# Optimization experiments

Hardware: AMD Instinct MI355X
Metric: run time of the kernel (lower is better)

Reference implementation:

```python
import jax, jax.numpy as jnp
import numpy as np

B, C, H, W = 4, 256, 64, 64
CP = C // 4  # embedding_channels, k=4 hardcoded
# branch index -> (key-stream i, query/value-stream j); streams: 0=t,1=b,2=m
IIDX = np.array([0, 0, 0, 1, 1, 1, 2, 2, 2])  # which stream feeds k
JIDX = np.array([0, 1, 2, 0, 1, 2, 0, 1, 2])  # which stream feeds q and v


def setup_inputs() -> dict:
    key = jax.random.key(0)
    ks = jax.random.split(key, 6)
    scale = 0.05
    return {
        "t": jax.random.normal(ks[0], (B, C, H, W), jnp.float32),
        "b": jax.random.normal(ks[1], (B, C, H, W), jnp.float32),
        "m": jax.random.normal(ks[2], (B, C, H, W), jnp.float32),
        "W_qkv": jax.random.normal(ks[3], (9, C, C), jnp.float32) * scale,
        "W_red": jax.random.normal(ks[4], (9, CP, C), jnp.float32) * scale,
        "W_rec": jax.random.normal(ks[5], (9, C, CP), jnp.float32) * scale,
    }


def _pool(x):
    # ChannelAttention: global avg pool + global max pool -> [B, C']
    return jnp.mean(x, axis=(2, 3)) + jnp.max(x, axis=(2, 3))


def _channel_attention(q, k, v, w_red, w_rec):
    # q,k,v: [B,C,H,W]; w_red: [C',C]; w_rec: [C,C']
    ori = q + k + v
    red = lambda x: jax.nn.relu(jnp.einsum("bchw,ec->behw", x, w_red))
    qr, kr, vr = red(q), red(k), red(v)
    f = _pool(kr)  # key   -> [B,C']
    g = _pool(qr)  # query -> [B,C']
    h = _pool(vr)  # value -> [B,C']
    # s = f^T g : [B,C',C']; softmax over dim=1 (rows), per torch nn.Softmax(dim=1)
    s = f[:, :, None] * g[:, None, :]
    beta = jax.nn.softmax(s, axis=1)
    vout = jnp.einsum("bi,bij->bj", h, beta)  # [B,C']
    # recovery 1x1 conv on [B,C',1,1]; bilinear upsample from 1x1 == broadcast
    o = jax.nn.sigmoid(jnp.einsum("be,ce->bc", vout, w_rec))  # [B,C]
    return o[:, :, None, None] * ori


def reference(t, b, m, W_qkv, W_red, W_rec):
    x = jnp.stack([t, b, m])  # [3,B,C,H,W]
    Wp = W_qkv.reshape(3, 3, C, C)  # [stream, (q,k,v), C_out, C_in]
    proj = jnp.einsum("sbchw,sjec->sjbehw", x, Wp)  # [3,3,B,C,H,W]
    Q, K, V = proj[:, 0], proj[:, 1], proj[:, 2]  # each [3,B,C,H,W]
    q9, k9, v9 = Q[JIDX], K[IIDX], V[JIDX]  # [9,B,C,H,W]
    outs = jax.vmap(_channel_attention)(q9, k9, v9, W_red, W_rec)
    return outs.sum(axis=0)
```

## Files before the change

### kernel.cpp

```cpp
#include <hip/hip_runtime.h>

#define Bn 4
#define Cn 256
#define HWn 4096
#define CPn 64
#define MP 640

typedef unsigned short u16;
typedef unsigned int u32;

using short8  = __attribute__((ext_vector_type(8))) short;
using floatx4 = __attribute__((ext_vector_type(4))) float;

static __device__ __forceinline__ u16 f2bf(float f) {
    union { float f; u32 u; } v; v.f = f;
    u32 r = (v.u + 0x7FFFu + ((v.u >> 16) & 1u)) >> 16;
    return (u16)r;
}

static __device__ __forceinline__ void gld16(const u16* g, u16* l) {
    __builtin_amdgcn_global_load_lds(
        (const __attribute__((address_space(1))) u32*)g,
        (__attribute__((address_space(3))) u32*)l, 16, 0, 0);
}


__global__ __launch_bounds__(256) void prep(
    const float* __restrict__ Tt, const float* __restrict__ Bt, const float* __restrict__ Mt,
    const float* __restrict__ Wqkv, const float* __restrict__ Wred,
    u16* __restrict__ xT, u16* __restrict__ CWp)
{
    __shared__ u16 T[64][72];
    __shared__ float As[16][64];
    __shared__ float Bs[16][64];
    const int t = threadIdx.x;

    if (blockIdx.z < 3) {
        const int s  = blockIdx.z, b = blockIdx.y;
        const int ct = blockIdx.x & 3, hwt = blockIdx.x >> 2;
        const int c0 = ct * 64, hw0 = hwt * 64;
        const float* X = (s == 0 ? Tt : (s == 1 ? Bt : Mt)) + (size_t)b * Cn * HWn;

        const int cl = t >> 2, q = t & 3;
        const float* src = X + (size_t)(c0 + cl) * HWn + hw0 + q * 16;
        #pragma unroll
        for (int u = 0; u < 4; ++u) {
            const float4 v = *(const float4*)(src + u * 4);
            T[cl][q * 16 + u * 4 + 0] = f2bf(v.x);
            T[cl][q * 16 + u * 4 + 1] = f2bf(v.y);
            T[cl][q * 16 + u * 4 + 2] = f2bf(v.z);
            T[cl][q * 16 + u * 4 + 3] = f2bf(v.w);
        }
        __syncthreads();

        const int wl = t >> 2;
        u16* dst = xT + ((size_t)((s * Bn + b) * HWn) + hw0 + wl) * Cn + c0 + q * 16;
        #pragma unroll
        for (int u = 0; u < 2; ++u) {
            u32 w0 = (u32)T[q * 16 + u * 8 + 0][wl] | ((u32)T[q * 16 + u * 8 + 1][wl] << 16);
            u32 w1 = (u32)T[q * 16 + u * 8 + 2][wl] | ((u32)T[q * 16 + u * 8 + 3][wl] << 16);
            u32 w2 = (u32)T[q * 16 + u * 8 + 4][wl] | ((u32)T[q * 16 + u * 8 + 5][wl] << 16);
            u32 w3 = (u32)T[q * 16 + u * 8 + 6][wl] | ((u32)T[q * 16 + u * 8 + 7][wl] << 16);
            uint4 pk = {w0, w1, w2, w3};
            *(uint4*)(dst + u * 8) = pk;
        }
        return;
    }

    const int lin = blockIdx.y * 256 + blockIdx.x;
    if (lin >= 108) return;
    const int c0  = (lin & 3) * 64;
    const int rest = lin >> 2;
    const int y9 = rest % 9, s = rest / 9;
    const int tt = y9 / 3, m3 = y9 % 3;
    const int idx = (tt == 1) ? (3 * s + m3) : (3 * m3 + s);

    const float* A  = Wred + (size_t)idx * CPn * Cn;
    const float* Bm = Wqkv + (size_t)(3 * s + tt) * Cn * Cn;

    const int ty = t >> 4, tx = t & 15;
    float acc[4][4] = {};

    for (int k0 = 0; k0 < Cn; k0 += 16) {
        {
            const int r = t >> 2, eq = (t & 3) * 4;
            const float4 a = *(const float4*)(A + (size_t)r * Cn + k0 + eq);
            As[eq + 0][r] = a.x; As[eq + 1][r] = a.y; As[eq + 2][r] = a.z; As[eq + 3][r] = a.w;
        }
        {
            const int r = t >> 4, cq = (t & 15) * 4;
            *(float4*)(&Bs[r][cq]) = *(const float4*)(Bm + (size_t)(k0 + r) * Cn + c0 + cq);
        }
        __syncthreads();
        #pragma unroll
        for (int k = 0; k < 16; ++k) {
            const float4 a4 = *(const float4*)(&As[k][ty * 4]);
            const float4 b4 = *(const float4*)(&Bs[k][tx * 4]);
            const float a[4] = {a4.x, a4.y, a4.z, a4.w};
            const float bb[4] = {b4.x, b4.y, b4.z, b4.w};
            #pragma unroll
            for (int i = 0; i < 4; ++i)
                #pragma unroll
                for (int j = 0; j < 4; ++j)
                    acc[i][j] = fmaf(a[i], bb[j], acc[i][j]);
        }
        __syncthreads();
    }

    u16* outp = CWp + (size_t)s * MP * Cn;
    #pragma unroll
    for (int i = 0; i < 4; ++i) {
        const int row = tt * 192 + m3 * 64 + ty * 4 + i;
        unsigned long long pk =
            (unsigned long long)f2bf(acc[i][0]) |
            ((unsigned long long)f2bf(acc[i][1]) << 16) |
            ((unsigned long long)f2bf(acc[i][2]) << 32) |
            ((unsigned long long)f2bf(acc[i][3]) << 48);
        *(unsigned long long*)(outp + (size_t)row * Cn + c0 + tx * 4) = pk;
    }
}

#define NSUB 16

__global__ __launch_bounds__(256, 1) void redpool_mfma(
    const u16* __restrict__ xT, const u16* __restrict__ CWp,
    float* __restrict__ Psum, float* __restrict__ Pmax)
{
    const int s   = blockIdx.z;
    const int mt  = blockIdx.x >> 4, nch = blockIdx.x & 15;
    const int m0  = mt * 128;
    const int nbase = nch * 1024;

    const u16* Ap = CWp + (size_t)s * MP * Cn;
    const u16* Bp = xT + (size_t)s * Bn * HWn * Cn;

    __shared__ __align__(16) u16 Bs[2][32 * 512];

    const int t = threadIdx.x;
    const int w = t >> 6, lane = t & 63;
    const int l15 = lane & 15, q = lane >> 4;
    const int wr = w >> 1, wc = w & 1;

    short8 af[4][8];
    {
        const u16* Arow = Ap + (size_t)(m0 + wr * 64 + l15) * Cn + q * 8;
        #pragma unroll
        for (int i = 0; i < 4; ++i)
            #pragma unroll
            for (int kk = 0; kk < 8; ++kk)
                af[i][kk] = *(const short8*)(Arow + (size_t)(i * 16) * Cn + kk * 32);
    }

    auto stageB = [&](int it, int buf) {
        const u16* Bsrc = Bp + (size_t)(nbase + it * 64 + l15) * Cn + q * 8;
        #pragma unroll
        for (int pi = 0; pi < 8; ++pi) {
            const int p = w * 8 + pi;
            gld16(Bsrc + (size_t)((p >> 3) * 16) * Cn + (p & 7) * 32, &Bs[buf][p * 512]);
        }
    };
    stageB(0, 0);

    float rs[4][4] = {};
    float rm[4][4] = {};

    for (int it = 0; it < NSUB; ++it) {
        __syncthreads();
        if (it + 1 < NSUB) stageB(it + 1, (it + 1) & 1);
        const u16* bb = Bs[it & 1];

        floatx4 acc[4][2] = {};
        #pragma unroll
        for (int kk = 0; kk < 8; ++kk) {
            short8 bf[2];
            #pragma unroll
            for (int j = 0; j < 2; ++j)
                bf[j] = *(const short8*)&bb[((wc * 2 + j) * 8 + kk) * 512 + lane * 8];
            #pragma unroll
            for (int i = 0; i < 4; ++i)
                #pragma unroll
                for (int j = 0; j < 2; ++j)
                    acc[i][j] = __builtin_amdgcn_mfma_f32_16x16x32_bf16(af[i][kk], bf[j], acc[i][j], 0, 0, 0);
        }
        #pragma unroll
        for (int i = 0; i < 4; ++i)
            #pragma unroll
            for (int r = 0; r < 4; ++r) {
                const float v0 = fmaxf(acc[i][0][r], 0.f);
                const float v1 = fmaxf(acc[i][1][r], 0.f);
                rs[i][r] += v0 + v1;
                rm[i][r] = fmaxf(rm[i][r], fmaxf(v0, v1));
            }
    }

    #pragma unroll
    for (int i = 0; i < 4; ++i)
        #pragma unroll
        for (int r = 0; r < 4; ++r) {
            #pragma unroll
            for (int off = 1; off < 16; off <<= 1) {
                rs[i][r] += __shfl_xor(rs[i][r], off);
                rm[i][r] = fmaxf(rm[i][r], __shfl_xor(rm[i][r], off));
            }
        }

    __syncthreads();
    float* Lsum = (float*)&Bs[0][0];
    float* Lmax = Lsum + 256;
    if (l15 == 0) {
        #pragma unroll
        for (int i = 0; i < 4; ++i)
            #pragma unroll
            for (int r = 0; r < 4; ++r) {
                const int row = wr * 64 + i * 16 + q * 4 + r;
                Lsum[wc * 128 + row] = rs[i][r];
                Lmax[wc * 128 + row] = rm[i][r];
            }
    }
    __syncthreads();
    if (t < 128) {
        const int R = m0 + t;
        const size_t o = ((size_t)s * MP + R) * 16 + nch;
        Psum[o] = Lsum[t] + Lsum[128 + t];
        Pmax[o] = fmaxf(Lmax[t], Lmax[128 + t]);
    }
}

__global__ __launch_bounds__(64) void attn_small(
    const float* __restrict__ Psum, const float* __restrict__ Pmax,
    float* __restrict__ vout)
{
    const int idx = blockIdx.x / Bn;
    const int bb  = blockIdx.x % Bn;
    __shared__ float ff[CPn], gg[CPn], hh[CPn];
    const int t = threadIdx.x;

    float v[3];
    #pragma unroll
    for (int tt = 0; tt < 3; ++tt) {
        const int s_ = (tt == 1) ? idx / 3 : idx % 3;
        const int m3 = (tt == 1) ? idx % 3 : idx / 3;
        const int R  = tt * 192 + m3 * 64 + t;
        const size_t base = ((size_t)s_ * MP + R) * 16 + bb * 4;
        float sm = 0.f, mx = 0.f;
        #pragma unroll
        for (int u = 0; u < 4; ++u) {
            sm += Psum[base + u];
            mx = fmaxf(mx, Pmax[base + u]);
        }
        v[tt] = sm * (1.0f / HWn) + mx;
    }
    gg[t] = v[0];
    ff[t] = v[1];
    hh[t] = v[2];
    __syncthreads();

    const float gj = gg[t];
    float mx = -1e30f;
    for (int i = 0; i < CPn; ++i) mx = fmaxf(mx, ff[i] * gj);
    float den = 0.f, num = 0.f;
    for (int i = 0; i < CPn; ++i) {
        const float e = expf(ff[i] * gj - mx);
        den += e;
        num += hh[i] * e;
    }
    vout[((size_t)idx * Bn + bb) * CPn + t] = num / den;
}

__global__ __launch_bounds__(256) void build_M(
    const float* __restrict__ Wqkv, const float* __restrict__ Wrec,
    const float* __restrict__ vout, u16* __restrict__ Mm)
{
    const int s = blockIdx.x >> 8, m = blockIdx.x & 255;
    const int b = blockIdx.y;
    const int t = threadIdx.x;
    __shared__ float cc[2];

    if (t < CPn) {
        float d[6];
        #pragma unroll
        for (int j = 0; j < 6; ++j) {
            const int idx = (j < 3) ? (s + 3 * j) : (3 * s + (j - 3));
            d[j] = vout[((size_t)idx * Bn + b) * CPn + t] *
                   Wrec[((size_t)idx * Cn + m) * CPn + t];
        }
        #pragma unroll
        for (int off = 32; off >= 1; off >>= 1)
            #pragma unroll
            for (int j = 0; j < 6; ++j)
                d[j] += __shfl_xor(d[j], off);
        if (t == 0) {
            float cA = 0.f, cK = 0.f;
            #pragma unroll
            for (int j = 0; j < 3; ++j) {
                cA += 1.0f / (1.0f + expf(-d[j]));
                cK += 1.0f / (1.0f + expf(-d[j + 3]));
            }
            cc[0] = cA; cc[1] = cK;
        }
    }
    __syncthreads();
    const float cA = cc[0], cK = cc[1];
    const float wq = Wqkv[((size_t)(3 * s + 0) * Cn + m) * Cn + t];
    const float wk = Wqkv[((size_t)(3 * s + 1) * Cn + m) * Cn + t];
    const float wv = Wqkv[((size_t)(3 * s + 2) * Cn + m) * Cn + t];
    Mm[((size_t)(b * 256 + m)) * 768 + s * 256 + t] = f2bf(cA * (wq + wv) + cK * wk);
}

__global__ __launch_bounds__(256, 1) void final_mfma(
    const u16* __restrict__ xT, const u16* __restrict__ Mm,
    float* __restrict__ out)
{
    const int b  = blockIdx.y;
    const int mt = blockIdx.x >> 5, nt = blockIdx.x & 31;
    const int m0 = mt * 128, n0 = nt * 128;

    __shared__ __align__(16) u16 As[2][32 * 512];
    __shared__ __align__(16) u16 Bs[2][32 * 512];

    const int t = threadIdx.x;
    const int w = t >> 6, lane = t & 63;
    const int l15 = lane & 15, q = lane >> 4;
    const int rb = (w >> 1) * 64, cb = (w & 1) * 64;

    auto stage = [&](int it, int buf) {
        const int k0 = it * 128;
        const int s = k0 >> 8, c0 = k0 & 255;
        const u16* Asrc = Mm + (size_t)(b * 256 + m0 + l15) * 768 + k0 + q * 8;
        const u16* Bsrc = xT + ((size_t)((s * Bn + b) * HWn) + n0 + l15) * Cn + c0 + q * 8;
        #pragma unroll
        for (int pi = 0; pi < 8; ++pi) {
            const int p = w * 8 + pi;
            const size_t roff = (size_t)((p >> 2) * 16);
            gld16(Asrc + roff * 768 + (p & 3) * 32, &As[buf][p * 512]);
            gld16(Bsrc + roff * Cn + (p & 3) * 32, &Bs[buf][p * 512]);
        }
    };
    stage(0, 0);

    floatx4 acc[4][4] = {};

    for (int it = 0; it < 6; ++it) {
        __syncthreads();
        if (it + 1 < 6) stage(it + 1, (it + 1) & 1);
        const u16* as = As[it & 1];
        const u16* bs = Bs[it & 1];
        #pragma unroll
        for (int kk = 0; kk < 4; ++kk) {
            short8 af[4], bf[4];
            #pragma unroll
            for (int i = 0; i < 4; ++i)
                af[i] = *(const short8*)&as[((((w >> 1) * 4 + i) << 2) + kk) * 512 + lane * 8];
            #pragma unroll
            for (int j = 0; j < 4; ++j)
                bf[j] = *(const short8*)&bs[((((w & 1) * 4 + j) << 2) + kk) * 512 + lane * 8];
            #pragma unroll
            for (int i = 0; i < 4; ++i)
                #pragma unroll
                for (int j = 0; j < 4; ++j)
                    acc[i][j] = __builtin_amdgcn_mfma_f32_16x16x32_bf16(af[i], bf[j], acc[i][j], 0, 0, 0);
        }
    }

    #pragma unroll
    for (int i = 0; i < 4; ++i)
        #pragma unroll
        for (int j = 0; j < 4; ++j)
            #pragma unroll
            for (int r = 0; r < 4; ++r) {
                const int row = m0 + rb + i * 16 + q * 4 + r;
                const int col = n0 + cb + j * 16 + l15;
                out[((size_t)(b * 256) + row) * HWn + col] = acc[i][j][r];
            }
}

extern "C" void kernel_launch(void* const* d_in, const int* in_sizes, int n_in,
                              void* d_out, int out_size, void* d_ws, size_t ws_size,
                              hipStream_t stream)
{
    const float* Tt   = (const float*)d_in[0];
    const float* Bt   = (const float*)d_in[1];
    const float* Mt   = (const float*)d_in[2];
    const float* Wqkv = (const float*)d_in[3];
    const float* Wred = (const float*)d_in[4];
    const float* Wrec = (const float*)d_in[5];
    float* out = (float*)d_out;

    unsigned char* p = (unsigned char*)d_ws;
    u16* xT = (u16*)p;            p += (size_t)3 * Bn * HWn * Cn * 2;
    u16* Mm = (u16*)p;            p += (size_t)Bn * 256 * 768 * 2;
    u16* CWp = (u16*)p;           p += (size_t)3 * MP * Cn * 2;
    float* Psum = (float*)p;      p += (size_t)3 * MP * 16 * 4;
    float* Pmax = (float*)p;      p += (size_t)3 * MP * 16 * 4;
    float* vout = (float*)p;      p += (size_t)9 * Bn * CPn * 4;

    prep        <<<dim3(256, Bn, 4), 256, 0, stream>>>(Tt, Bt, Mt, Wqkv, Wred, xT, CWp);
    redpool_mfma<<<dim3(80, 1, 3),   256, 0, stream>>>(xT, CWp, Psum, Pmax);
    attn_small  <<<9 * Bn,            64, 0, stream>>>(Psum, Pmax, vout);
    build_M     <<<dim3(768, Bn),    256, 0, stream>>>(Wqkv, Wrec, vout, Mm);
    final_mfma  <<<dim3(64, Bn),     256, 0, stream>>>(xT, Mm, out);
}
```

Measured before the change: 170.3 us.

## Fuse input bf16 transpose with reduction-pool MFMA into a single pass

Splits the weight-composition GEMM into its own small kernel and merges the fp32-to-bf16 transpose of the inputs with the reduce+ReLU+pool MFMA stage. Each block converts a 128-pixel slice, writes xT for the final stage, and also lays the tile out in LDS panes that feed the MFMAs directly. This removes the global re-read of xT that the separate pool kernel needed. In exchange each block recomputes over all 640 rows with A fragments reloaded from global per tile, and the partial-pool buffers grow to 128 slots, so attn_small does more reduction work. The pool kernel also launches fewer blocks (384 instead of 240 plus the prep grid).

```diff
diff --git a/kernel.cpp b/kernel.cpp
--- a/kernel.cpp
+++ b/kernel.cpp
@@ -25,59 +25,22 @@
 }
 
 
-__global__ __launch_bounds__(256) void prep(
-    const float* __restrict__ Tt, const float* __restrict__ Bt, const float* __restrict__ Mt,
+__global__ __launch_bounds__(256) void compose_red(
     const float* __restrict__ Wqkv, const float* __restrict__ Wred,
-    u16* __restrict__ xT, u16* __restrict__ CWp)
-{
-    __shared__ u16 T[64][72];
+    u16* __restrict__ CWp)
+{
+    const int c0 = blockIdx.x * 64;
+    const int y  = blockIdx.y;
+    const int s  = y / 9, y9 = y % 9;
+    const int tt = y9 / 3, m3 = y9 % 3;
+    const int idx = (tt == 1) ? (3 * s + m3) : (3 * m3 + s);
+
+    const float* A  = Wred + (size_t)idx * CPn * Cn;
+    const float* Bm = Wqkv + (size_t)(3 * s + tt) * Cn * Cn;
+
     __shared__ float As[16][64];
     __shared__ float Bs[16][64];
     const int t = threadIdx.x;
-
-    if (blockIdx.z < 3) {
-        const int s  = blockIdx.z, b = blockIdx.y;
-        const int ct = blockIdx.x & 3, hwt = blockIdx.x >> 2;
-        const int c0 = ct * 64, hw0 = hwt * 64;
-        const float* X = (s == 0 ? Tt : (s == 1 ? Bt : Mt)) + (size_t)b * Cn * HWn;
-
-        const int cl = t >> 2, q = t & 3;
-        const float* src = X + (size_t)(c0 + cl) * HWn + hw0 + q * 16;
-        #pragma unroll
-        for (int u = 0; u < 4; ++u) {
-            const float4 v = *(const float4*)(src + u * 4);
-            T[cl][q * 16 + u * 4 + 0] = f2bf(v.x);
-            T[cl][q * 16 + u * 4 + 1] = f2bf(v.y);
-            T[cl][q * 16 + u * 4 + 2] = f2bf(v.z);
-            T[cl][q * 16 + u * 4 + 3] = f2bf(v.w);
-        }
-        __syncthreads();
-
-        const int wl = t >> 2;
-        u16* dst = xT + ((size_t)((s * Bn + b) * HWn) + hw0 + wl) * Cn + c0 + q * 16;
-        #pragma unroll
-        for (int u = 0; u < 2; ++u) {
-            u32 w0 = (u32)T[q * 16 + u * 8 + 0][wl] | ((u32)T[q * 16 + u * 8 + 1][wl] << 16);
-            u32 w1 = (u32)T[q * 16 + u * 8 + 2][wl] | ((u32)T[q * 16 + u * 8 + 3][wl] << 16);
-            u32 w2 = (u32)T[q * 16 + u * 8 + 4][wl] | ((u32)T[q * 16 + u * 8 + 5][wl] << 16);
-            u32 w3 = (u32)T[q * 16 + u * 8 + 6][wl] | ((u32)T[q * 16 + u * 8 + 7][wl] << 16);
-            uint4 pk = {w0, w1, w2, w3};
-            *(uint4*)(dst + u * 8) = pk;
-        }
-        return;
-    }
-
-    const int lin = blockIdx.y * 256 + blockIdx.x;
-    if (lin >= 108) return;
-    const int c0  = (lin & 3) * 64;
-    const int rest = lin >> 2;
-    const int y9 = rest % 9, s = rest / 9;
-    const int tt = y9 / 3, m3 = y9 % 3;
-    const int idx = (tt == 1) ? (3 * s + m3) : (3 * m3 + s);
-
-    const float* A  = Wred + (size_t)idx * CPn * Cn;
-    const float* Bm = Wqkv + (size_t)(3 * s + tt) * Cn * Cn;
-
     const int ty = t >> 4, tx = t & 15;
     float acc[4][4] = {};
 
@@ -120,109 +83,139 @@
     }
 }
 
-#define NSUB 16
-
-__global__ __launch_bounds__(256, 1) void redpool_mfma(
-    const u16* __restrict__ xT, const u16* __restrict__ CWp,
-    float* __restrict__ Psum, float* __restrict__ Pmax)
+__global__ __launch_bounds__(256, 2) void pass1(
+    const float* __restrict__ Tt, const float* __restrict__ Bt, const float* __restrict__ Mt,
+    const u16* __restrict__ CWp,
+    u16* __restrict__ xT, float* __restrict__ Psum, float* __restrict__ Pmax)
 {
     const int s   = blockIdx.z;
-    const int mt  = blockIdx.x >> 4, nch = blockIdx.x & 15;
-    const int m0  = mt * 128;
-    const int nbase = nch * 1024;
-
+    const int nch = blockIdx.x;
+    const int b   = nch >> 5;
+    const int hwb = (nch & 31) * 128;
+
+    const float* X = (s == 0 ? Tt : (s == 1 ? Bt : Mt)) + (size_t)b * Cn * HWn;
     const u16* Ap = CWp + (size_t)s * MP * Cn;
-    const u16* Bp = xT + (size_t)s * Bn * HWn * Cn;
-
-    __shared__ __align__(16) u16 Bs[2][32 * 512];
+    u16* xTb = xT + (size_t)((s * Bn + b) * HWn) * Cn;
+
+    __shared__ u16 T[64][72];
+    __shared__ __align__(16) u16 panes[32 * 512];
 
     const int t = threadIdx.x;
     const int w = t >> 6, lane = t & 63;
     const int l15 = lane & 15, q = lane >> 4;
-    const int wr = w >> 1, wc = w & 1;
-
-    short8 af[4][8];
+    const int cl = t >> 2, q4 = t & 3;
+
+    float rs[5][2][4] = {};
+    float rm[5][2][4] = {};
+
+    float4 v[2][4];
     {
-        const u16* Arow = Ap + (size_t)(m0 + wr * 64 + l15) * Cn + q * 8;
-        #pragma unroll
-        for (int i = 0; i < 4; ++i)
-            #pragma unroll
-            for (int kk = 0; kk < 8; ++kk)
-                af[i][kk] = *(const short8*)(Arow + (size_t)(i * 16) * Cn + kk * 32);
-    }
-
-    auto stageB = [&](int it, int buf) {
-        const u16* Bsrc = Bp + (size_t)(nbase + it * 64 + l15) * Cn + q * 8;
-        #pragma unroll
-        for (int pi = 0; pi < 8; ++pi) {
-            const int p = w * 8 + pi;
-            gld16(Bsrc + (size_t)((p >> 3) * 16) * Cn + (p & 7) * 32, &Bs[buf][p * 512]);
-        }
-    };
-    stageB(0, 0);
-
-    float rs[4][4] = {};
-    float rm[4][4] = {};
-
-    for (int it = 0; it < NSUB; ++it) {
-        __syncthreads();
-        if (it + 1 < NSUB) stageB(it + 1, (it + 1) & 1);
-        const u16* bb = Bs[it & 1];
-
-        floatx4 acc[4][2] = {};
-        #pragma unroll
-        for (int kk = 0; kk < 8; ++kk) {
-            short8 bf[2];
-            #pragma unroll
-            for (int j = 0; j < 2; ++j)
-                bf[j] = *(const short8*)&bb[((wc * 2 + j) * 8 + kk) * 512 + lane * 8];
-            #pragma unroll
-            for (int i = 0; i < 4; ++i)
-                #pragma unroll
-                for (int j = 0; j < 2; ++j)
-                    acc[i][j] = __builtin_amdgcn_mfma_f32_16x16x32_bf16(af[i][kk], bf[j], acc[i][j], 0, 0, 0);
-        }
-        #pragma unroll
-        for (int i = 0; i < 4; ++i)
+        const float* src = X + (size_t)cl * HWn + hwb + q4 * 16;
+        #pragma unroll
+        for (int u = 0; u < 4; ++u) v[0][u] = *(const float4*)(src + u * 4);
+    }
+
+    for (int ph = 0; ph < 8; ++ph) {
+        const int st = ph >> 2, ct = ph & 3;
+        const int cur = ph & 1;
+        __syncthreads();
+        if (ph < 7) {
+            const int st2 = (ph + 1) >> 2, ct2 = (ph + 1) & 3;
+            const float* src = X + (size_t)(ct2 * 64 + cl) * HWn + hwb + st2 * 64 + q4 * 16;
+            #pragma unroll
+            for (int u = 0; u < 4; ++u) v[cur ^ 1][u] = *(const float4*)(src + u * 4);
+        }
+        #pragma unroll
+        for (int u = 0; u < 4; ++u) {
+            T[cl][q4 * 16 + u * 4 + 0] = f2bf(v[cur][u].x);
+            T[cl][q4 * 16 + u * 4 + 1] = f2bf(v[cur][u].y);
+            T[cl][q4 * 16 + u * 4 + 2] = f2bf(v[cur][u].z);
+            T[cl][q4 * 16 + u * 4 + 3] = f2bf(v[cur][u].w);
+        }
+        __syncthreads();
+        {
+            const int wl  = t >> 2;
+            const int hw0 = hwb + st * 64;
+            #pragma unroll
+            for (int u2 = 0; u2 < 2; ++u2) {
+                const int cb = q4 * 16 + u2 * 8;
+                u32 w0 = (u32)T[cb + 0][wl] | ((u32)T[cb + 1][wl] << 16);
+                u32 w1 = (u32)T[cb + 2][wl] | ((u32)T[cb + 3][wl] << 16);
+                u32 w2 = (u32)T[cb + 4][wl] | ((u32)T[cb + 5][wl] << 16);
+                u32 w3 = (u32)T[cb + 6][wl] | ((u32)T[cb + 7][wl] << 16);
+                uint4 pk = {w0, w1, w2, w3};
+                const int c = ct * 64 + cb;
+                *(uint4*)(xTb + (size_t)(hw0 + wl) * Cn + c) = pk;
+                const int p = (wl >> 4) * 8 + (c >> 5);
+                const int cquad = (c >> 3) & 3;
+                *(uint4*)(&panes[(p * 64 + cquad * 16 + (wl & 15)) * 8]) = pk;
+            }
+        }
+        if (ct == 3) {
+            __syncthreads();
+            #pragma unroll
+            for (int mt = 0; mt < 5; ++mt) {
+                short8 af[2][8];
+                const u16* Arow = Ap + (size_t)(mt * 128 + w * 32 + l15) * Cn + q * 8;
+                #pragma unroll
+                for (int i = 0; i < 2; ++i)
+                    #pragma unroll
+                    for (int kk = 0; kk < 8; ++kk)
+                        af[i][kk] = *(const short8*)(Arow + (size_t)(i * 16) * Cn + kk * 32);
+                floatx4 acc[2][4] = {};
+                #pragma unroll
+                for (int kk = 0; kk < 8; ++kk) {
+                    short8 bf[4];
+                    #pragma unroll
+                    for (int j = 0; j < 4; ++j)
+                        bf[j] = *(const short8*)&panes[((j * 8 + kk) * 64 + lane) * 8];
+                    #pragma unroll
+                    for (int i = 0; i < 2; ++i)
+                        #pragma unroll
+                        for (int j = 0; j < 4; ++j)
+                            acc[i][j] = __builtin_amdgcn_mfma_f32_16x16x32_bf16(af[i][kk], bf[j], acc[i][j], 0, 0, 0);
+                }
+                #pragma unroll
+                for (int i = 0; i < 2; ++i)
+                    #pragma unroll
+                    for (int r = 0; r < 4; ++r) {
+                        float sm = 0.f, mx = 0.f;
+                        #pragma unroll
+                        for (int j = 0; j < 4; ++j) {
+                            const float vv = fmaxf(acc[i][j][r], 0.f);
+                            sm += vv; mx = fmaxf(mx, vv);
+                        }
+                        rs[mt][i][r] += sm;
+                        rm[mt][i][r] = fmaxf(rm[mt][i][r], mx);
+                    }
+            }
+        }
+    }
+
+    #pragma unroll
+    for (int mt = 0; mt < 5; ++mt)
+        #pragma unroll
+        for (int i = 0; i < 2; ++i)
             #pragma unroll
             for (int r = 0; r < 4; ++r) {
-                const float v0 = fmaxf(acc[i][0][r], 0.f);
-                const float v1 = fmaxf(acc[i][1][r], 0.f);
-                rs[i][r] += v0 + v1;
-                rm[i][r] = fmaxf(rm[i][r], fmaxf(v0, v1));
-            }
-    }
-
-    #pragma unroll
-    for (int i = 0; i < 4; ++i)
-        #pragma unroll
-        for (int r = 0; r < 4; ++r) {
-            #pragma unroll
-            for (int off = 1; off < 16; off <<= 1) {
-                rs[i][r] += __shfl_xor(rs[i][r], off);
-                rm[i][r] = fmaxf(rm[i][r], __shfl_xor(rm[i][r], off));
-            }
-        }
-
-    __syncthreads();
-    float* Lsum = (float*)&Bs[0][0];
-    float* Lmax = Lsum + 256;
+                #pragma unroll
+                for (int off = 1; off < 16; off <<= 1) {
+                    rs[mt][i][r] += __shfl_xor(rs[mt][i][r], off);
+                    rm[mt][i][r] = fmaxf(rm[mt][i][r], __shfl_xor(rm[mt][i][r], off));
+                }
+            }
     if (l15 == 0) {
         #pragma unroll
-        for (int i = 0; i < 4; ++i)
-            #pragma unroll
-            for (int r = 0; r < 4; ++r) {
-                const int row = wr * 64 + i * 16 + q * 4 + r;
-                Lsum[wc * 128 + row] = rs[i][r];
-                Lmax[wc * 128 + row] = rm[i][r];
-            }
-    }
-    __syncthreads();
-    if (t < 128) {
-        const int R = m0 + t;
-        const size_t o = ((size_t)s * MP + R) * 16 + nch;
-        Psum[o] = Lsum[t] + Lsum[128 + t];
-        Pmax[o] = fmaxf(Lmax[t], Lmax[128 + t]);
+        for (int mt = 0; mt < 5; ++mt)
+            #pragma unroll
+            for (int i = 0; i < 2; ++i)
+                #pragma unroll
+                for (int r = 0; r < 4; ++r) {
+                    const int R = mt * 128 + w * 32 + i * 16 + q * 4 + r;
+                    const size_t o = ((size_t)s * MP + R) * 128 + nch;
+                    Psum[o] = rs[mt][i][r];
+                    Pmax[o] = rm[mt][i][r];
+                }
     }
 }
 
@@ -241,10 +234,10 @@
         const int s_ = (tt == 1) ? idx / 3 : idx % 3;
         const int m3 = (tt == 1) ? idx % 3 : idx / 3;
         const int R  = tt * 192 + m3 * 64 + t;
-        const size_t base = ((size_t)s_ * MP + R) * 16 + bb * 4;
+        const size_t base = ((size_t)s_ * MP + R) * 128 + bb * 32;
         float sm = 0.f, mx = 0.f;
         #pragma unroll
-        for (int u = 0; u < 4; ++u) {
+        for (int u = 0; u < 32; ++u) {
             sm += Psum[base + u];
             mx = fmaxf(mx, Pmax[base + u]);
         }
@@ -390,13 +383,13 @@
     u16* xT = (u16*)p;            p += (size_t)3 * Bn * HWn * Cn * 2;
     u16* Mm = (u16*)p;            p += (size_t)Bn * 256 * 768 * 2;
     u16* CWp = (u16*)p;           p += (size_t)3 * MP * Cn * 2;
-    float* Psum = (float*)p;      p += (size_t)3 * MP * 16 * 4;
-    float* Pmax = (float*)p;      p += (size_t)3 * MP * 16 * 4;
+    float* Psum = (float*)p;      p += (size_t)3 * MP * 128 * 4;
+    float* Pmax = (float*)p;      p += (size_t)3 * MP * 128 * 4;
     float* vout = (float*)p;      p += (size_t)9 * Bn * CPn * 4;
 
-    prep        <<<dim3(256, Bn, 4), 256, 0, stream>>>(Tt, Bt, Mt, Wqkv, Wred, xT, CWp);
-    redpool_mfma<<<dim3(80, 1, 3),   256, 0, stream>>>(xT, CWp, Psum, Pmax);
-    attn_small  <<<9 * Bn,            64, 0, stream>>>(Psum, Pmax, vout);
-    build_M     <<<dim3(768, Bn),    256, 0, stream>>>(Wqkv, Wrec, vout, Mm);
-    final_mfma  <<<dim3(64, Bn),     256, 0, stream>>>(xT, Mm, out);
-}
+    compose_red<<<dim3(4, 27),     256, 0, stream>>>(Wqkv, Wred, CWp);
+    pass1      <<<dim3(128, 1, 3), 256, 0, stream>>>(Tt, Bt, Mt, CWp, xT, Psum, Pmax);
+    attn_small <<<9 * Bn,           64, 0, stream>>>(Psum, Pmax, vout);
+    build_M    <<<dim3(768, Bn),   256, 0, stream>>>(Wqkv, Wrec, vout, Mm);
+    final_mfma <<<dim3(64, Bn),    256, 0, stream>>>(xT, Mm, out);
+}
```

Result: slower. 279.2 us (+63.9%).
